# Kernel optimization log

Hardware: AMD Instinct MI355X
Metric: run time of the kernel (lower is better)

The kernel has to match this reference:

```python
import jax, jax.numpy as jnp
import numpy as np

NUM_HEADS = 16

def setup_inputs() -> dict:
    key = jax.random.key(0)
    ks = jax.random.split(key, 12)
    B, NQ, NK = 4, 1024, 1024
    DQ = DK = DV = 1024
    AH = 1024   # num_heads * head_dim
    OUT = 1024
    s = lambda d: 1.0 / np.sqrt(d)
    return {
        "q": jax.random.normal(ks[0], (B, NQ, DQ), jnp.float32),
        "k": jax.random.normal(ks[1], (B, NK, DK), jnp.float32),
        "v": jax.random.normal(ks[2], (B, NK, DV), jnp.float32),
        "attn_mask": jnp.ones((NQ, NK), jnp.float32),
        "Wq": jax.random.normal(ks[3], (DQ, AH), jnp.float32) * s(DQ),
        "bq": jnp.zeros((AH,), jnp.float32),
        "Wk": jax.random.normal(ks[4], (DK, AH), jnp.float32) * s(DK),
        "bk": jnp.zeros((AH,), jnp.float32),
        "Wv": jax.random.normal(ks[5], (DV, AH), jnp.float32) * s(DV),
        "bv": jnp.zeros((AH,), jnp.float32),
        "Wo": jax.random.normal(ks[6], (AH, OUT), jnp.float32) * s(AH),
        "bo": jnp.zeros((OUT,), jnp.float32),
    }

def reference(q, k, v, attn_mask, Wq, bq, Wk, bk, Wv, bv, Wo, bo):
    b, n_q, _ = q.shape
    n_k = k.shape[1]
    all_head_dim = Wq.shape[1]
    scale = all_head_dim ** (-0.5)  # NOTE: module scales by all_head_dim, not head_dim

    # module reshapes as (b, n, head_dim, num_heads): heads are the LAST axis
    def split_heads(x):
        return x.reshape(b, x.shape[1], -1, NUM_HEADS).transpose(0, 3, 1, 2)  # (b,H,n,d)

    qh = split_heads(q @ Wq + bq) * scale
    kh = split_heads(k @ Wk + bk)
    vh = split_heads(v @ Wv + bv)

    attn = jnp.einsum('bhqd,bhkd->bhqk', qh, kh)
    attn = attn - 100000000.0 * (1.0 - attn_mask[None, None, :, :])
    attn = jax.nn.softmax(attn, axis=-1)

    o = jnp.einsum('bhqk,bhkd->bhqd', attn, vh)
    o = o.transpose(0, 2, 3, 1).reshape(b, n_q, -1)  # (b,n_q,head_dim*H)
    return o @ Wo + bo
```

## Files before the change

kernel.cpp:

```cpp
#include <hip/hip_runtime.h>
#include <stdint.h>

typedef __attribute__((ext_vector_type(8))) short short8;
typedef __attribute__((ext_vector_type(8))) unsigned short ushort8;
typedef __attribute__((ext_vector_type(4))) float f32x4;
typedef unsigned short u16;
typedef unsigned int u32;

__device__ __forceinline__ u16 f2bf(float f){
  u32 u = __builtin_bit_cast(u32, f);
  u32 r = (u + 0x7fffu + ((u >> 16) & 1u)) >> 16;
  return (u16)r;
}

__device__ __forceinline__ void gload16(const void* g, void* l){
  __builtin_amdgcn_global_load_lds((const __attribute__((address_space(1))) void*)g,
                                   (__attribute__((address_space(3))) void*)l, 16, 0, 0);
}

__global__ void prep_kernel(const float* __restrict__ q, const float* __restrict__ k,
                            const float* __restrict__ v, u16* __restrict__ xq,
                            u16* __restrict__ xk, u16* __restrict__ xv,
                            const float* __restrict__ Wq, const float* __restrict__ Wk,
                            const float* __restrict__ Wv, const float* __restrict__ Wo,
                            u16* __restrict__ WqT, u16* __restrict__ WkT,
                            u16* __restrict__ WvT, u16* __restrict__ WoT){
  __shared__ float t[64][65];
  int bid = blockIdx.x;
  int tid = threadIdx.x;
  if (bid < 2048){
    const int NV8 = 4194304 / 8;
    for (int i = bid * 256 + tid; i < 3 * NV8; i += 2048 * 256){
      int tt = i / NV8, r = i - tt * NV8;
      const float4* src = (const float4*)(tt == 0 ? q : (tt == 1 ? k : v));
      u16* dst = (tt == 0 ? xq : (tt == 1 ? xk : xv));
      float4 f0 = src[r * 2], f1 = src[r * 2 + 1];
      ushort8 o;
      o[0] = f2bf(f0.x); o[1] = f2bf(f0.y); o[2] = f2bf(f0.z); o[3] = f2bf(f0.w);
      o[4] = f2bf(f1.x); o[5] = f2bf(f1.y); o[6] = f2bf(f1.z); o[7] = f2bf(f1.w);
      *(ushort8*)(dst + r * 8) = o;
    }
  } else {
    int idx = bid - 2048;
    int bx = idx & 15, by = (idx >> 4) & 15, z = idx >> 8;
    const float* src = (z == 0 ? Wq : (z == 1 ? Wk : (z == 2 ? Wv : Wo)));
    u16* dst = (z == 0 ? WqT : (z == 1 ? WkT : (z == 2 ? WvT : WoT)));
    int c0 = by * 64;
    #pragma unroll
    for (int p = 0; p < 4; ++p){
      int rl = p * 16 + (tid >> 4);
      int srcRow = (z < 3) ? (bx * 64 + rl) : (rl * 16 + bx);
      float4 f = *(const float4*)(src + srcRow * 1024 + c0 + (tid & 15) * 4);
      t[rl][(tid & 15) * 4 + 0] = f.x;
      t[rl][(tid & 15) * 4 + 1] = f.y;
      t[rl][(tid & 15) * 4 + 2] = f.z;
      t[rl][(tid & 15) * 4 + 3] = f.w;
    }
    __syncthreads();
    int ro = tid >> 2;
    int kc = (tid & 3) * 16;
    int outBase = (c0 + ro) * 1024 + bx * 64;
    #pragma unroll
    for (int j = 0; j < 16; ++j)
      dst[outBase + kc + j] = f2bf(t[kc + j][ro]);
  }
}

__global__ void maskflag_kernel(const float* __restrict__ mask, u32* __restrict__ flags){
  int q0 = blockIdx.x * 128, k0 = blockIdx.y * 64;
  int tid = threadIdx.x;
  bool ok = true;
  #pragma unroll
  for (int p = 0; p < 8; ++p){
    int fi = p * 256 + tid;
    int r = fi >> 4, c = (fi & 15) * 4;
    float4 f = *(const float4*)(mask + (size_t)(q0 + r) * 1024 + k0 + c);
    ok = ok && (f.x == 1.0f) && (f.y == 1.0f) && (f.z == 1.0f) && (f.w == 1.0f);
  }
  __shared__ int s_ok[4];
  unsigned long long b = __ballot(ok);
  if ((tid & 63) == 0) s_ok[tid >> 6] = (b == ~0ull) ? 1 : 0;
  __syncthreads();
  if (tid == 0)
    flags[blockIdx.x * 16 + blockIdx.y] = (u32)(s_ok[0] & s_ok[1] & s_ok[2] & s_ok[3]);
}

struct QkvArgs {
  const u16* A[3]; const u16* BT[3]; const float* bias[3];
  u16* outQ; u16* outK; u16* outVT;
};

__global__ __launch_bounds__(256, 3)
void gemm_qkv_kernel(QkvArgs args){
  __shared__ __align__(16) u16 As[3][128 * 32];
  __shared__ __align__(16) u16 Bs[3][128 * 32];
  int wg = blockIdx.x;
  int l  = (wg & 7) * 96 + (wg >> 3);
  int z  = l >> 8;
  int rem = l & 255;
  int m0 = (rem >> 3) * 128, n0 = (rem & 7) * 128;
  const u16* __restrict__ A  = args.A[z];
  const u16* __restrict__ BT = args.BT[z];
  const float* __restrict__ bias = args.bias[z];
  int tid = threadIdx.x, w = tid >> 6, lane = tid & 63, lr = lane & 15, lg = lane >> 4;
  int wr = w >> 1, wc = w & 1;
  f32x4 acc[4][4];
  #pragma unroll
  for (int i = 0; i < 4; ++i)
    #pragma unroll
    for (int j = 0; j < 4; ++j)
      acc[i][j] = f32x4{0.f, 0.f, 0.f, 0.f};

  auto stage = [&](int kt, int b){
    int k0 = kt * 32;
    #pragma unroll
    for (int p = 0; p < 2; ++p){
      int chunk = p * 4096 + w * 1024;
      int L = chunk + lane * 16;
      int row = L >> 6, inrow = L & 63;
      int srcB = inrow ^ (((row >> 1) & 3) << 4);
      gload16(A + (m0 + row) * 1024 + k0 + (srcB >> 1), (char*)As[b] + chunk);
      gload16(BT + (n0 + row) * 1024 + k0 + (srcB >> 1), (char*)Bs[b] + chunk);
    }
  };
  stage(0, 0);
  stage(1, 1);

  for (int kt = 0; kt < 32; ++kt){
    int cur = kt % 3;
    if (kt < 30){
      stage(kt + 2, (kt + 2) % 3);
      asm volatile("s_waitcnt vmcnt(8)" ::: "memory");
    } else if (kt == 30){
      asm volatile("s_waitcnt vmcnt(4)" ::: "memory");
    } else {
      asm volatile("s_waitcnt vmcnt(0)" ::: "memory");
    }
    __builtin_amdgcn_s_barrier();

    short8 af[4], bfr[4];
    int cb = lg * 16;
    #pragma unroll
    for (int i = 0; i < 4; ++i){
      int ra = wr * 64 + i * 16 + lr;
      af[i] = *(const short8*)((const char*)As[cur] + ra * 64 + (cb ^ (((ra >> 1) & 3) << 4)));
      int rb = wc * 64 + i * 16 + lr;
      bfr[i] = *(const short8*)((const char*)Bs[cur] + rb * 64 + (cb ^ (((rb >> 1) & 3) << 4)));
    }
    #pragma unroll
    for (int i = 0; i < 4; ++i)
      #pragma unroll
      for (int j = 0; j < 4; ++j)
        acc[i][j] = __builtin_amdgcn_mfma_f32_16x16x32_bf16(af[i], bfr[j], acc[i][j], 0, 0, 0);

    __builtin_amdgcn_s_barrier();
  }

  float bv[4];
  #pragma unroll
  for (int j = 0; j < 4; ++j) bv[j] = bias[n0 + wc * 64 + j * 16 + lr];
  float scale = (z == 0) ? 0.03125f : 1.0f;
  int bb = m0 >> 10;
  int dd0 = (n0 + wc * 64) >> 4;
  if (z == 2){
    #pragma unroll
    for (int i = 0; i < 4; ++i){
      int nn0 = (m0 + wr * 64 + i * 16 + lg * 4) & 1023;
      #pragma unroll
      for (int j = 0; j < 4; ++j){
        ushort4 pw;
        pw.x = f2bf((acc[i][j][0] + bv[j]) * scale);
        pw.y = f2bf((acc[i][j][1] + bv[j]) * scale);
        pw.z = f2bf((acc[i][j][2] + bv[j]) * scale);
        pw.w = f2bf((acc[i][j][3] + bv[j]) * scale);
        *(ushort4*)(args.outVT + ((size_t)(bb * 16 + lr) * 64 + dd0 + j) * 1024 + nn0) = pw;
      }
    }
  } else {
    u16* o = (z == 0) ? args.outQ : args.outK;
    #pragma unroll
    for (int i = 0; i < 4; ++i){
      #pragma unroll
      for (int rr = 0; rr < 4; ++rr){
        int nn = (m0 + wr * 64 + i * 16 + lg * 4 + rr) & 1023;
        ushort4 pw;
        pw.x = f2bf((acc[i][0][rr] + bv[0]) * scale);
        pw.y = f2bf((acc[i][1][rr] + bv[1]) * scale);
        pw.z = f2bf((acc[i][2][rr] + bv[2]) * scale);
        pw.w = f2bf((acc[i][3][rr] + bv[3]) * scale);
        *(ushort4*)(o + ((size_t)(bb * 16 + lr) * 1024 + nn) * 64 + dd0) = pw;
      }
    }
  }
}

__global__ __launch_bounds__(256, 2)
void attn_kernel(const u16* __restrict__ Qh, const u16* __restrict__ Kh,
                 const u16* __restrict__ VT, const float* __restrict__ mask,
                 const u32* __restrict__ flags, u16* __restrict__ Oh){
  __shared__ __align__(16) u16 Qs[128 * 64];
  __shared__ __align__(16) u16 Ks[2][64 * 64];
  __shared__ __align__(16) u16 Vs[2][64 * 64];
  __shared__ __align__(16) u16 Ps[128 * 72];
  int tid = threadIdx.x, w = tid >> 6, lane = tid & 63, lr = lane & 15, lg = lane >> 4;
  int wg = blockIdx.x;
  int idx = wg >> 3;
  int bh = (wg & 7) * 8 + (idx >> 3);
  int qt = idx & 7;
  int q0 = qt * 128;
  const u16* Qb = Qh + (size_t)bh * 65536;
  const u16* Kb = Kh + (size_t)bh * 65536;
  const u16* Vb = VT + (size_t)bh * 65536;

  u32 fbits = 0;
  #pragma unroll
  for (int t = 0; t < 16; ++t) fbits |= (flags[qt * 16 + t] & 1u) << t;

  #pragma unroll
  for (int r = 0; r < 4; ++r){
    int chunk = (r * 4 + w) * 1024;
    int L = chunk + lane * 16;
    int row = L >> 7, inrow = L & 127;
    int srcB = inrow ^ ((row & 7) << 4);
    gload16(Qb + (q0 + row) * 64 + (srcB >> 1), (char*)Qs + chunk);
  }

  auto stage_kv = [&](int t, int b){
    int kn = t * 64;
    #pragma unroll
    for (int r = 0; r < 2; ++r){
      int chunk = (r * 4 + w) * 1024;
      int L = chunk + lane * 16;
      int row = L >> 7, inrow = L & 127;
      int srcB = inrow ^ ((row & 7) << 4);
      gload16(Kb + (kn + row) * 64 + (srcB >> 1), (char*)Ks[b] + chunk);
      gload16(Vb + row * 1024 + kn + (srcB >> 1), (char*)Vs[b] + chunk);
    }
  };
  stage_kv(0, 0);

  f32x4 o[2][4];
  float m_run[2], l_run[2];
  m_run[0] = m_run[1] = -3.0e38f;
  l_run[0] = l_run[1] = 0.f;
  #pragma unroll
  for (int i = 0; i < 2; ++i)
    #pragma unroll
    for (int j = 0; j < 4; ++j)
      o[i][j] = f32x4{0.f, 0.f, 0.f, 0.f};

  for (int kt = 0; kt < 16; ++kt){
    int cur = kt & 1;
    int kn0 = kt * 64;

    f32x4 s[2][4];
    if (fbits & (1u << kt)){
      #pragma unroll
      for (int i = 0; i < 2; ++i)
        #pragma unroll
        for (int j = 0; j < 4; ++j)
          s[i][j] = f32x4{0.f, 0.f, 0.f, 0.f};
    } else {
      #pragma unroll
      for (int i = 0; i < 2; ++i){
        int qg = q0 + w * 32 + i * 16 + lr;
        #pragma unroll
        for (int j = 0; j < 4; ++j){
          int kg = kn0 + j * 16 + lg * 4;
          float4 mm = *(const float4*)(mask + (size_t)qg * 1024 + kg);
          s[i][j][0] = fmaf(100000000.0f, mm.x, -100000000.0f);
          s[i][j][1] = fmaf(100000000.0f, mm.y, -100000000.0f);
          s[i][j][2] = fmaf(100000000.0f, mm.z, -100000000.0f);
          s[i][j][3] = fmaf(100000000.0f, mm.w, -100000000.0f);
        }
      }
    }

    if (kt < 15){
      stage_kv(kt + 1, cur ^ 1);
      asm volatile("s_waitcnt vmcnt(4)" ::: "memory");
    } else {
      asm volatile("s_waitcnt vmcnt(0)" ::: "memory");
    }
    __builtin_amdgcn_s_barrier();

    #pragma unroll
    for (int kh = 0; kh < 2; ++kh){
      short8 qf[2], kf[4];
      int cb = kh * 64 + lg * 16;
      #pragma unroll
      for (int i = 0; i < 2; ++i){
        int ra = w * 32 + i * 16 + lr;
        qf[i] = *(const short8*)((const char*)Qs + ra * 128 + (cb ^ ((ra & 7) << 4)));
      }
      #pragma unroll
      for (int j = 0; j < 4; ++j){
        int rb = j * 16 + lr;
        kf[j] = *(const short8*)((const char*)Ks[cur] + rb * 128 + (cb ^ ((rb & 7) << 4)));
      }
      #pragma unroll
      for (int i = 0; i < 2; ++i)
        #pragma unroll
        for (int j = 0; j < 4; ++j)
          s[i][j] = __builtin_amdgcn_mfma_f32_16x16x32_bf16(kf[j], qf[i], s[i][j], 0, 0, 0);
    }

    float alpha[2];
    #pragma unroll
    for (int i = 0; i < 2; ++i){
      float m0a = fmaxf(fmaxf(s[i][0][0], s[i][0][1]), fmaxf(s[i][0][2], s[i][0][3]));
      float m1a = fmaxf(fmaxf(s[i][1][0], s[i][1][1]), fmaxf(s[i][1][2], s[i][1][3]));
      float m2a = fmaxf(fmaxf(s[i][2][0], s[i][2][1]), fmaxf(s[i][2][2], s[i][2][3]));
      float m3a = fmaxf(fmaxf(s[i][3][0], s[i][3][1]), fmaxf(s[i][3][2], s[i][3][3]));
      float mx = fmaxf(fmaxf(m0a, m1a), fmaxf(m2a, m3a));
      mx = fmaxf(mx, __shfl_xor(mx, 16));
      mx = fmaxf(mx, __shfl_xor(mx, 32));
      float mnew = fmaxf(m_run[i], mx);
      alpha[i] = __expf(m_run[i] - mnew);
      m_run[i] = mnew;
      float rs = 0.f;
      #pragma unroll
      for (int j = 0; j < 4; ++j)
        #pragma unroll
        for (int rr = 0; rr < 4; ++rr){
          float p = __expf(s[i][j][rr] - mnew);
          s[i][j][rr] = p;
          rs += p;
        }
      rs += __shfl_xor(rs, 16);
      rs += __shfl_xor(rs, 32);
      l_run[i] = l_run[i] * alpha[i] + rs;
      int prow = w * 32 + i * 16 + lr;
      #pragma unroll
      for (int j = 0; j < 4; ++j){
        ushort4 pw;
        pw.x = f2bf(s[i][j][0]); pw.y = f2bf(s[i][j][1]);
        pw.z = f2bf(s[i][j][2]); pw.w = f2bf(s[i][j][3]);
        *(ushort4*)(Ps + prow * 72 + j * 16 + lg * 4) = pw;
      }
    }

    #pragma unroll
    for (int i = 0; i < 2; ++i)
      #pragma unroll
      for (int jd = 0; jd < 4; ++jd)
        #pragma unroll
        for (int rr = 0; rr < 4; ++rr)
          o[i][jd][rr] *= alpha[i];

    #pragma unroll
    for (int kh = 0; kh < 2; ++kh){
      short8 pf[2], vf[4];
      int cb = kh * 64 + lg * 16;
      #pragma unroll
      for (int i = 0; i < 2; ++i){
        int ra = w * 32 + i * 16 + lr;
        pf[i] = *(const short8*)((const char*)Ps + ra * 144 + cb);
      }
      #pragma unroll
      for (int jd = 0; jd < 4; ++jd){
        int rb = jd * 16 + lr;
        vf[jd] = *(const short8*)((const char*)Vs[cur] + rb * 128 + (cb ^ ((rb & 7) << 4)));
      }
      #pragma unroll
      for (int i = 0; i < 2; ++i)
        #pragma unroll
        for (int jd = 0; jd < 4; ++jd)
          o[i][jd] = __builtin_amdgcn_mfma_f32_16x16x32_bf16(vf[jd], pf[i], o[i][jd], 0, 0, 0);
    }
    __builtin_amdgcn_s_barrier();
  }

  #pragma unroll
  for (int i = 0; i < 2; ++i){
    float inv = 1.0f / l_run[i];
    int qg = q0 + w * 32 + i * 16 + lr;
    #pragma unroll
    for (int jd = 0; jd < 4; ++jd){
      ushort4 ov;
      ov.x = f2bf(o[i][jd][0] * inv);
      ov.y = f2bf(o[i][jd][1] * inv);
      ov.z = f2bf(o[i][jd][2] * inv);
      ov.w = f2bf(o[i][jd][3] * inv);
      *(ushort4*)(Oh + ((size_t)bh * 1024 + qg) * 64 + jd * 16 + lg * 4) = ov;
    }
  }
}

__global__ __launch_bounds__(256, 4)
void gemm_out_kernel(const u16* __restrict__ Oh, const u16* __restrict__ WoT,
                     const float* __restrict__ bo, float* __restrict__ out){
  __shared__ __align__(16) u16 As[3][128 * 32];
  __shared__ __align__(16) u16 Bs[3][64 * 32];
  int wg = blockIdx.x;
  int l  = (wg & 7) * 64 + (wg >> 3);
  int m0 = (l >> 4) * 128, n0 = (l & 15) * 64;
  int tid = threadIdx.x, w = tid >> 6, lane = tid & 63, lr = lane & 15, lg = lane >> 4;
  int wm = w >> 1, wn = w & 1;
  f32x4 acc[4][2];
  #pragma unroll
  for (int i = 0; i < 4; ++i)
    #pragma unroll
    for (int j = 0; j < 2; ++j)
      acc[i][j] = f32x4{0.f, 0.f, 0.f, 0.f};

  auto stage = [&](int kt, int b){
    int hh = kt >> 1;
    int dofs = (kt & 1) * 32;
    int k0 = kt * 32;
    #pragma unroll
    for (int p = 0; p < 2; ++p){
      int chunk = p * 4096 + w * 1024;
      int L = chunk + lane * 16;
      int row = L >> 6, inrow = L & 63;
      int srcB = inrow ^ (((row >> 1) & 3) << 4);
      int m = m0 + row;
      int bb = m >> 10, nn = m & 1023;
      gload16(Oh + ((size_t)(bb * 16 + hh) * 1024 + nn) * 64 + dofs + (srcB >> 1),
              (char*)As[b] + chunk);
    }
    {
      int chunk = w * 1024;
      int L = chunk + lane * 16;
      int row = L >> 6, inrow = L & 63;
      int srcB = inrow ^ (((row >> 1) & 3) << 4);
      gload16(WoT + (n0 + row) * 1024 + k0 + (srcB >> 1), (char*)Bs[b] + chunk);
    }
  };
  stage(0, 0);
  stage(1, 1);

  for (int kt = 0; kt < 32; ++kt){
    int cur = kt % 3;
    if (kt < 30){
      stage(kt + 2, (kt + 2) % 3);
      asm volatile("s_waitcnt vmcnt(6)" ::: "memory");
    } else if (kt == 30){
      asm volatile("s_waitcnt vmcnt(3)" ::: "memory");
    } else {
      asm volatile("s_waitcnt vmcnt(0)" ::: "memory");
    }
    __builtin_amdgcn_s_barrier();

    short8 af[4], bfr[2];
    int cb = lg * 16;
    #pragma unroll
    for (int i = 0; i < 4; ++i){
      int ra = wm * 64 + i * 16 + lr;
      af[i] = *(const short8*)((const char*)As[cur] + ra * 64 + (cb ^ (((ra >> 1) & 3) << 4)));
    }
    #pragma unroll
    for (int j = 0; j < 2; ++j){
      int rb = wn * 32 + j * 16 + lr;
      bfr[j] = *(const short8*)((const char*)Bs[cur] + rb * 64 + (cb ^ (((rb >> 1) & 3) << 4)));
    }
    #pragma unroll
    for (int i = 0; i < 4; ++i)
      #pragma unroll
      for (int j = 0; j < 2; ++j)
        acc[i][j] = __builtin_amdgcn_mfma_f32_16x16x32_bf16(af[i], bfr[j], acc[i][j], 0, 0, 0);

    __builtin_amdgcn_s_barrier();
  }

  float bv[2];
  #pragma unroll
  for (int j = 0; j < 2; ++j) bv[j] = bo[n0 + wn * 32 + j * 16 + lr];
  #pragma unroll
  for (int i = 0; i < 4; ++i)
    #pragma unroll
    for (int j = 0; j < 2; ++j){
      int gcol = n0 + wn * 32 + j * 16 + lr;
      #pragma unroll
      for (int rr = 0; rr < 4; ++rr){
        int grow = m0 + wm * 64 + i * 16 + lg * 4 + rr;
        out[(size_t)grow * 1024 + gcol] = acc[i][j][rr] + bv[j];
      }
    }
}

extern "C" void kernel_launch(void* const* d_in, const int* in_sizes, int n_in,
                              void* d_out, int out_size, void* d_ws, size_t ws_size,
                              hipStream_t stream){
  const float* q    = (const float*)d_in[0];
  const float* k    = (const float*)d_in[1];
  const float* v    = (const float*)d_in[2];
  const float* mask = (const float*)d_in[3];
  const float* Wq   = (const float*)d_in[4];
  const float* bq   = (const float*)d_in[5];
  const float* Wk   = (const float*)d_in[6];
  const float* bk   = (const float*)d_in[7];
  const float* Wv   = (const float*)d_in[8];
  const float* bv   = (const float*)d_in[9];
  const float* Wo   = (const float*)d_in[10];
  const float* bo   = (const float*)d_in[11];

  char* ws = (char*)d_ws;
  u16* Qh  = (u16*)(ws + (size_t)0);
  u16* Kh  = (u16*)(ws + ((size_t)8  << 20));
  u16* VT  = (u16*)(ws + ((size_t)16 << 20));
  u16* Oh  = (u16*)(ws + ((size_t)24 << 20));
  u16* Xq  = (u16*)(ws + ((size_t)32 << 20));
  u16* Xk  = (u16*)(ws + ((size_t)40 << 20));
  u16* Xv  = (u16*)(ws + ((size_t)48 << 20));
  u16* WqT = (u16*)(ws + ((size_t)56 << 20));
  u16* WkT = (u16*)(ws + ((size_t)58 << 20));
  u16* WvT = (u16*)(ws + ((size_t)60 << 20));
  u16* WoT = (u16*)(ws + ((size_t)62 << 20));
  u32* Flags = (u32*)(ws + ((size_t)32 << 20));

  prep_kernel<<<dim3(3072), dim3(256), 0, stream>>>(q, k, v, Xq, Xk, Xv,
                                                    Wq, Wk, Wv, Wo, WqT, WkT, WvT, WoT);

  QkvArgs a;
  a.A[0] = Xq;  a.A[1] = Xk;  a.A[2] = Xv;
  a.BT[0] = WqT; a.BT[1] = WkT; a.BT[2] = WvT;
  a.bias[0] = bq; a.bias[1] = bk; a.bias[2] = bv;
  a.outQ = Qh; a.outK = Kh; a.outVT = VT;
  gemm_qkv_kernel<<<dim3(768), dim3(256), 0, stream>>>(a);

  maskflag_kernel<<<dim3(8, 16), dim3(256), 0, stream>>>(mask, Flags);
  attn_kernel<<<dim3(512), dim3(256), 0, stream>>>(Qh, Kh, VT, mask, Flags, Oh);
  gemm_out_kernel<<<dim3(512), dim3(256), 0, stream>>>(Oh, WoT, bo, (float*)d_out);
}
```

Before: 125.4 us.

## Retile QKV GEMM, hoist Q fragments, use exp2 with lazy rescale in attention

```diff
diff --git a/kernel.cpp b/kernel.cpp
--- a/kernel.cpp
+++ b/kernel.cpp
@@ -90,25 +90,25 @@
   u16* outQ; u16* outK; u16* outVT;
 };
 
-__global__ __launch_bounds__(256, 3)
+__global__ __launch_bounds__(256, 6)
 void gemm_qkv_kernel(QkvArgs args){
-  __shared__ __align__(16) u16 As[3][128 * 32];
-  __shared__ __align__(16) u16 Bs[3][128 * 32];
+  __shared__ __align__(16) u16 As[2][128 * 32];
+  __shared__ __align__(16) u16 Bs[2][64 * 32];
   int wg = blockIdx.x;
-  int l  = (wg & 7) * 96 + (wg >> 3);
-  int z  = l >> 8;
-  int rem = l & 255;
-  int m0 = (rem >> 3) * 128, n0 = (rem & 7) * 128;
+  int l  = (wg & 7) * 192 + (wg >> 3);
+  int z  = l >> 9;
+  int rem = l & 511;
+  int m0 = (rem >> 4) * 128, n0 = (rem & 15) * 64;
   const u16* __restrict__ A  = args.A[z];
   const u16* __restrict__ BT = args.BT[z];
   const float* __restrict__ bias = args.bias[z];
   int tid = threadIdx.x, w = tid >> 6, lane = tid & 63, lr = lane & 15, lg = lane >> 4;
-  int wr = w >> 1, wc = w & 1;
-  f32x4 acc[4][4];
+  int wm = w >> 1, wn = w & 1;
+  f32x4 acc[4][2];
   #pragma unroll
   for (int i = 0; i < 4; ++i)
     #pragma unroll
-    for (int j = 0; j < 4; ++j)
+    for (int j = 0; j < 2; ++j)
       acc[i][j] = f32x4{0.f, 0.f, 0.f, 0.f};
 
   auto stage = [&](int kt, int b){
@@ -120,59 +120,65 @@
       int row = L >> 6, inrow = L & 63;
       int srcB = inrow ^ (((row >> 1) & 3) << 4);
       gload16(A + (m0 + row) * 1024 + k0 + (srcB >> 1), (char*)As[b] + chunk);
+    }
+    {
+      int chunk = w * 1024;
+      int L = chunk + lane * 16;
+      int row = L >> 6, inrow = L & 63;
+      int srcB = inrow ^ (((row >> 1) & 3) << 4);
       gload16(BT + (n0 + row) * 1024 + k0 + (srcB >> 1), (char*)Bs[b] + chunk);
     }
   };
   stage(0, 0);
-  stage(1, 1);
 
   for (int kt = 0; kt < 32; ++kt){
-    int cur = kt % 3;
-    if (kt < 30){
-      stage(kt + 2, (kt + 2) % 3);
-      asm volatile("s_waitcnt vmcnt(8)" ::: "memory");
-    } else if (kt == 30){
-      asm volatile("s_waitcnt vmcnt(4)" ::: "memory");
+    int cur = kt & 1;
+    if (kt < 31){
+      stage(kt + 1, cur ^ 1);
+      asm volatile("s_waitcnt vmcnt(3)" ::: "memory");
     } else {
       asm volatile("s_waitcnt vmcnt(0)" ::: "memory");
     }
     __builtin_amdgcn_s_barrier();
 
-    short8 af[4], bfr[4];
+    short8 af[4], bfr[2];
     int cb = lg * 16;
     #pragma unroll
     for (int i = 0; i < 4; ++i){
-      int ra = wr * 64 + i * 16 + lr;
+      int ra = wm * 64 + i * 16 + lr;
       af[i] = *(const short8*)((const char*)As[cur] + ra * 64 + (cb ^ (((ra >> 1) & 3) << 4)));
-      int rb = wc * 64 + i * 16 + lr;
-      bfr[i] = *(const short8*)((const char*)Bs[cur] + rb * 64 + (cb ^ (((rb >> 1) & 3) << 4)));
+    }
+    #pragma unroll
+    for (int j = 0; j < 2; ++j){
+      int rb = wn * 32 + j * 16 + lr;
+      bfr[j] = *(const short8*)((const char*)Bs[cur] + rb * 64 + (cb ^ (((rb >> 1) & 3) << 4)));
     }
     #pragma unroll
     for (int i = 0; i < 4; ++i)
       #pragma unroll
-      for (int j = 0; j < 4; ++j)
+      for (int j = 0; j < 2; ++j)
         acc[i][j] = __builtin_amdgcn_mfma_f32_16x16x32_bf16(af[i], bfr[j], acc[i][j], 0, 0, 0);
 
     __builtin_amdgcn_s_barrier();
   }
 
-  float bv[4];
-  #pragma unroll
-  for (int j = 0; j < 4; ++j) bv[j] = bias[n0 + wc * 64 + j * 16 + lr];
-  float scale = (z == 0) ? 0.03125f : 1.0f;
+  float bv[2];
+  #pragma unroll
+  for (int j = 0; j < 2; ++j) bv[j] = bias[n0 + wn * 32 + j * 16 + lr];
+  float scale = (z == 0) ? 0.0450842200f : 1.0f;
   int bb = m0 >> 10;
-  int dd0 = (n0 + wc * 64) >> 4;
+  int dd0 = (n0 + wn * 32) >> 4;
   if (z == 2){
     #pragma unroll
     for (int i = 0; i < 4; ++i){
-      int nn0 = (m0 + wr * 64 + i * 16 + lg * 4) & 1023;
-      #pragma unroll
-      for (int j = 0; j < 4; ++j){
+      int nn0 = (m0 + wm * 64 + i * 16 + lg * 4) & 1023;
+      #pragma unroll
+      for (int j = 0; j < 2; ++j){
         ushort4 pw;
-        pw.x = f2bf((acc[i][j][0] + bv[j]) * scale);
-        pw.y = f2bf((acc[i][j][1] + bv[j]) * scale);
-        pw.z = f2bf((acc[i][j][2] + bv[j]) * scale);
-        pw.w = f2bf((acc[i][j][3] + bv[j]) * scale);
+        pw.x = f2bf(acc[i][j][0] + bv[j]);
+        pw.y = f2bf(acc[i][j][1] + bv[j]);
+        pw.z = f2bf(acc[i][j][2] + bv[j]);
+        pw.w = f2bf(acc[i][j][3] + bv[j]);
         *(ushort4*)(args.outVT + ((size_t)(bb * 16 + lr) * 64 + dd0 + j) * 1024 + nn0) = pw;
       }
     }
@@ -182,13 +188,11 @@
     for (int i = 0; i < 4; ++i){
       #pragma unroll
       for (int rr = 0; rr < 4; ++rr){
-        int nn = (m0 + wr * 64 + i * 16 + lg * 4 + rr) & 1023;
-        ushort4 pw;
-        pw.x = f2bf((acc[i][0][rr] + bv[0]) * scale);
-        pw.y = f2bf((acc[i][1][rr] + bv[1]) * scale);
-        pw.z = f2bf((acc[i][2][rr] + bv[2]) * scale);
-        pw.w = f2bf((acc[i][3][rr] + bv[3]) * scale);
-        *(ushort4*)(o + ((size_t)(bb * 16 + lr) * 1024 + nn) * 64 + dd0) = pw;
+        int nn = (m0 + wm * 64 + i * 16 + lg * 4 + rr) & 1023;
+        u16 p0 = f2bf((acc[i][0][rr] + bv[0]) * scale);
+        u16 p1 = f2bf((acc[i][1][rr] + bv[1]) * scale);
+        u32 pk = (u32)p0 | ((u32)p1 << 16);
+        *(u32*)(o + ((size_t)(bb * 16 + lr) * 1024 + nn) * 64 + dd0) = pk;
       }
     }
   }
@@ -239,6 +243,18 @@
   };
   stage_kv(0, 0);
 
+  asm volatile("s_waitcnt vmcnt(4)" ::: "memory");
+  __builtin_amdgcn_s_barrier();
+  short8 qreg[2][2];
+  #pragma unroll
+  for (int i = 0; i < 2; ++i)
+    #pragma unroll
+    for (int kh = 0; kh < 2; ++kh){
+      int ra = w * 32 + i * 16 + lr;
+      qreg[i][kh] = *(const short8*)((const char*)Qs + ra * 128 +
+                                     ((kh * 64 + lg * 16) ^ ((ra & 7) << 4)));
+    }
+
   f32x4 o[2][4];
   float m_run[2], l_run[2];
   m_run[0] = m_run[1] = -3.0e38f;
@@ -268,10 +284,10 @@
         for (int j = 0; j < 4; ++j){
           int kg = kn0 + j * 16 + lg * 4;
           float4 mm = *(const float4*)(mask + (size_t)qg * 1024 + kg);
-          s[i][j][0] = fmaf(100000000.0f, mm.x, -100000000.0f);
-          s[i][j][1] = fmaf(100000000.0f, mm.y, -100000000.0f);
-          s[i][j][2] = fmaf(100000000.0f, mm.z, -100000000.0f);
-          s[i][j][3] = fmaf(100000000.0f, mm.w, -100000000.0f);
+          s[i][j][0] = fmaf(1.44269504e8f, mm.x, -1.44269504e8f);
+          s[i][j][1] = fmaf(1.44269504e8f, mm.y, -1.44269504e8f);
+          s[i][j][2] = fmaf(1.44269504e8f, mm.z, -1.44269504e8f);
+          s[i][j][3] = fmaf(1.44269504e8f, mm.w, -1.44269504e8f);
         }
       }
     }
@@ -286,13 +302,8 @@
 
     #pragma unroll
     for (int kh = 0; kh < 2; ++kh){
-      short8 qf[2], kf[4];
+      short8 kf[4];
       int cb = kh * 64 + lg * 16;
-      #pragma unroll
-      for (int i = 0; i < 2; ++i){
-        int ra = w * 32 + i * 16 + lr;
-        qf[i] = *(const short8*)((const char*)Qs + ra * 128 + (cb ^ ((ra & 7) << 4)));
-      }
       #pragma unroll
       for (int j = 0; j < 4; ++j){
         int rb = j * 16 + lr;
@@ -302,10 +313,11 @@
       for (int i = 0; i < 2; ++i)
         #pragma unroll
         for (int j = 0; j < 4; ++j)
-          s[i][j] = __builtin_amdgcn_mfma_f32_16x16x32_bf16(kf[j], qf[i], s[i][j], 0, 0, 0);
+          s[i][j] = __builtin_amdgcn_mfma_f32_16x16x32_bf16(kf[j], qreg[i][kh], s[i][j], 0, 0, 0);
     }
 
     float alpha[2];
+    bool need[2];
     #pragma unroll
     for (int i = 0; i < 2; ++i){
       float m0a = fmaxf(fmaxf(s[i][0][0], s[i][0][1]), fmaxf(s[i][0][2], s[i][0][3]));
@@ -315,21 +327,28 @@
       float mx = fmaxf(fmaxf(m0a, m1a), fmaxf(m2a, m3a));
       mx = fmaxf(mx, __shfl_xor(mx, 16));
       mx = fmaxf(mx, __shfl_xor(mx, 32));
-      float mnew = fmaxf(m_run[i], mx);
-      alpha[i] = __expf(m_run[i] - mnew);
-      m_run[i] = mnew;
+      need[i] = __any(mx > m_run[i] + 8.0f);
+      float mnew;
+      if (need[i]){
+        mnew = fmaxf(m_run[i], mx);
+        alpha[i] = exp2f(m_run[i] - mnew);
+        m_run[i] = mnew;
+      } else {
+        mnew = m_run[i];
+        alpha[i] = 1.0f;
+      }
       float rs = 0.f;
       #pragma unroll
       for (int j = 0; j < 4; ++j)
         #pragma unroll
         for (int rr = 0; rr < 4; ++rr){
-          float p = __expf(s[i][j][rr] - mnew);
+          float p = exp2f(s[i][j][rr] - mnew);
           s[i][j][rr] = p;
           rs += p;
         }
       rs += __shfl_xor(rs, 16);
       rs += __shfl_xor(rs, 32);
-      l_run[i] = l_run[i] * alpha[i] + rs;
+      l_run[i] = need[i] ? (l_run[i] * alpha[i] + rs) : (l_run[i] + rs);
       int prow = w * 32 + i * 16 + lr;
       #pragma unroll
       for (int j = 0; j < 4; ++j){
@@ -342,11 +361,13 @@
 
     #pragma unroll
     for (int i = 0; i < 2; ++i)
-      #pragma unroll
-      for (int jd = 0; jd < 4; ++jd)
+      if (need[i]){
         #pragma unroll
-        for (int rr = 0; rr < 4; ++rr)
-          o[i][jd][rr] *= alpha[i];
+        for (int jd = 0; jd < 4; ++jd)
+          #pragma unroll
+          for (int rr = 0; rr < 4; ++rr)
+            o[i][jd][rr] *= alpha[i];
+      }
 
     #pragma unroll
     for (int kh = 0; kh < 2; ++kh){
@@ -390,8 +411,8 @@
 __global__ __launch_bounds__(256, 4)
 void gemm_out_kernel(const u16* __restrict__ Oh, const u16* __restrict__ WoT,
                      const float* __restrict__ bo, float* __restrict__ out){
-  __shared__ __align__(16) u16 As[3][128 * 32];
-  __shared__ __align__(16) u16 Bs[3][64 * 32];
+  __shared__ __align__(16) u16 As[4][128 * 32];
+  __shared__ __align__(16) u16 Bs[4][64 * 32];
   int wg = blockIdx.x;
   int l  = (wg & 7) * 64 + (wg >> 3);
   int m0 = (l >> 4) * 128, n0 = (l & 15) * 64;
@@ -429,11 +450,11 @@
   };
   stage(0, 0);
   stage(1, 1);
+  stage(2, 2);
 
   for (int kt = 0; kt < 32; ++kt){
-    int cur = kt % 3;
-    if (kt < 30){
-      stage(kt + 2, (kt + 2) % 3);
+    int cur = kt & 3;
+    if (kt <= 29){
       asm volatile("s_waitcnt vmcnt(6)" ::: "memory");
     } else if (kt == 30){
       asm volatile("s_waitcnt vmcnt(3)" ::: "memory");
@@ -454,13 +475,13 @@
       int rb = wn * 32 + j * 16 + lr;
       bfr[j] = *(const short8*)((const char*)Bs[cur] + rb * 64 + (cb ^ (((rb >> 1) & 3) << 4)));
     }
+    if (kt < 29) stage(kt + 3, (kt + 3) & 3);
+
     #pragma unroll
     for (int i = 0; i < 4; ++i)
       #pragma unroll
       for (int j = 0; j < 2; ++j)
         acc[i][j] = __builtin_amdgcn_mfma_f32_16x16x32_bf16(af[i], bfr[j], acc[i][j], 0, 0, 0);
-
-    __builtin_amdgcn_s_barrier();
   }
 
   float bv[2];
@@ -517,7 +538,7 @@
   a.BT[0] = WqT; a.BT[1] = WkT; a.BT[2] = WvT;
   a.bias[0] = bq; a.bias[1] = bk; a.bias[2] = bv;
   a.outQ = Qh; a.outK = Kh; a.outVT = VT;
-  gemm_qkv_kernel<<<dim3(768), dim3(256), 0, stream>>>(a);
+  gemm_qkv_kernel<<<dim3(1536), dim3(256), 0, stream>>>(a);
 
   maskflag_kernel<<<dim3(8, 16), dim3(256), 0, stream>>>(mask, Flags);
   attn_kernel<<<dim3(512), dim3(256), 0, stream>>>(Qh, Kh, VT, mask, Flags, Oh);
```

After: 152.6 us. 1.22x slower.
